# Performance work log

Hardware: AMD Instinct MI355X
Metric: run time of the kernel (lower is better)

Reference implementation:

```python
import jax, jax.numpy as jnp
import numpy as np

N = 50000      # nodes
E = 600000     # directed edges (before self-loops)
IN = 256       # in_channels
H = 4          # heads
C = 32         # hidden_channels (per head)
OUT = 64       # out_channels


def setup_inputs() -> dict:
    key = jax.random.key(0)
    ks = jax.random.split(key, 10)
    x = jax.random.normal(ks[0], (N, IN), dtype=jnp.float32)
    edge_index = jax.random.randint(ks[1], (2, E), 0, N, dtype=jnp.int64)
    W1 = jax.random.normal(ks[2], (IN, H * C), dtype=jnp.float32) / np.float32(np.sqrt(IN))
    a_src1 = jax.random.normal(ks[3], (H, C), dtype=jnp.float32) * 0.1
    a_dst1 = jax.random.normal(ks[4], (H, C), dtype=jnp.float32) * 0.1
    b1 = jnp.zeros((H * C,), dtype=jnp.float32)
    W2 = jax.random.normal(ks[5], (H * C, OUT), dtype=jnp.float32) / np.float32(np.sqrt(H * C))
    a_src2 = jax.random.normal(ks[6], (1, OUT), dtype=jnp.float32) * 0.1
    a_dst2 = jax.random.normal(ks[7], (1, OUT), dtype=jnp.float32) * 0.1
    b2 = jnp.zeros((OUT,), dtype=jnp.float32)
    return dict(x=x, edge_index=edge_index, W1=W1, a_src1=a_src1, a_dst1=a_dst1,
                b1=b1, W2=W2, a_src2=a_src2, a_dst2=a_dst2, b2=b2)


def gat_conv(x, src, dst, W, a_s, a_d, b, concat):
    """PyG GATConv (eval mode, self-loops already appended to src/dst).
    x: [N, F_in]; W: [F_in, H*C]; a_s, a_d: [H, C]; b: [H*C] or [C].
    Messages flow src (j) -> dst (i); softmax over incoming edges of dst."""
    heads, c = a_s.shape
    h = (x @ W).reshape(-1, heads, c)                      # [N, H, C]
    al_s = jnp.einsum('nhc,hc->nh', h, a_s)                # per-node src term
    al_d = jnp.einsum('nhc,hc->nh', h, a_d)                # per-node dst term
    e = jax.nn.leaky_relu(al_s[src] + al_d[dst], 0.2)      # [E, H]
    m = jax.ops.segment_max(e, dst, num_segments=N)        # stable segment softmax
    p = jnp.exp(e - m[dst])
    s = jax.ops.segment_sum(p, dst, num_segments=N)
    alpha = p / s[dst]                                     # [E, H]
    out = jax.ops.segment_sum(alpha[:, :, None] * h[src], dst, num_segments=N)  # [N, H, C]
    out = out.reshape(-1, heads * c) if concat else out.mean(axis=1)
    return out + b


def reference(x, edge_index, W1, a_src1, a_dst1, b1, W2, a_src2, a_dst2, b2):
    loops = jnp.arange(N, dtype=edge_index.dtype)          # PyG add_self_loops=True
    src = jnp.concatenate([edge_index[0], loops])
    dst = jnp.concatenate([edge_index[1], loops])
    h = gat_conv(x, src, dst, W1, a_src1, a_dst1, b1, concat=True)
    h = jax.nn.leaky_relu(h, 0.2)
    return gat_conv(h, src, dst, W2, a_src2, a_dst2, b2, concat=False)
```

## Files before the change

### kernel.cpp

```cpp
#include <hip/hip_runtime.h>
#include <hip/hip_bf16.h>

#define N_NODES 50000
#define E_EDGES 600000
#define F_IN    256
#define HC1     128
#define F_OUT   64
#define NBKT    196
#define BMAX    6144
#define APB     8192
#define NAB     80
#define GB1     1563
#define NPACK   (F_IN * HC1 + HC1 * F_OUT)

typedef __bf16 bf16x8 __attribute__((ext_vector_type(8)));
typedef __bf16 bf16x4 __attribute__((ext_vector_type(4)));
typedef float  f32x4  __attribute__((ext_vector_type(4)));

__device__ __forceinline__ float lrelu(float x) { return x > 0.f ? x : 0.2f * x; }
__device__ __forceinline__ float bfhi(unsigned v) { return __uint_as_float(v & 0xffff0000u); }
__device__ __forceinline__ float bflo(unsigned v) { return __uint_as_float(v << 16); }


__global__ __launch_bounds__(256) void init_kernel(const float* __restrict__ W1,
                                                   const float* __restrict__ W2,
                                                   __bf16* __restrict__ hi1, __bf16* __restrict__ lo1,
                                                   __bf16* __restrict__ hi2, __bf16* __restrict__ lo2,
                                                   int* __restrict__ bcur) {
    if (blockIdx.x == 0) {
        if (threadIdx.x < NBKT) bcur[threadIdx.x] = 0;
        return;
    }
    int tid = (blockIdx.x - 1) * 256 + threadIdx.x;
    if (tid >= NPACK) return;
    if (tid < F_IN * HC1) {
        int t = tid;
        int j = t & 7, l = (t >> 3) & 63, kt = (t >> 9) & 7, ct = t >> 12;
        int k = kt * 32 + (l >> 4) * 8 + j;
        int col = ct * 16 + (l & 15);
        float v = W1[k * HC1 + col];
        __bf16 h = (__bf16)v;
        hi1[t] = h;
        lo1[t] = (__bf16)(v - (float)h);
    } else {
        int t = tid - F_IN * HC1;
        int j = t & 7, l = (t >> 3) & 63, kt = (t >> 9) & 3, ct = t >> 11;
        int k = kt * 32 + (l >> 4) * 8 + j;
        int col = ct * 16 + (l & 15);
        float v = W2[k * F_OUT + col];
        __bf16 h = (__bf16)v;
        hi2[t] = h;
        lo2[t] = (__bf16)(v - (float)h);
    }
}


__global__ __launch_bounds__(256) void gemm1_bappend_kernel(
        const float* __restrict__ A,
        const __bf16* __restrict__ Whi, const __bf16* __restrict__ Wlo,
        const float* __restrict__ a_s, const float* __restrict__ a_d,
        __bf16* __restrict__ Cout, float* __restrict__ als, float* __restrict__ ald,
        const int* __restrict__ ei, int* __restrict__ bcur, int2* __restrict__ bstage) {
    __shared__ __bf16 ah[32][F_IN + 8];
    __shared__ __bf16 al[32][F_IN + 8];
    __shared__ int lcnt[NBKT];
    int tid = threadIdx.x;

    if (blockIdx.x < NAB) {
        const int TOT = E_EDGES + N_NODES;
        int bb = (int)blockIdx.x;
        int e0 = bb * APB;
        int e1 = e0 + APB < TOT ? e0 + APB : TOT;
        if (tid < NBKT) lcnt[tid] = 0;
        __syncthreads();
        for (int i = e0 + tid; i < e1; i += 256) {
            int d = (i < E_EDGES) ? ei[E_EDGES + i] : (i - E_EDGES);
            atomicAdd(&lcnt[d >> 8], 1);
        }
        __syncthreads();
        if (tid < NBKT) {
            int c = lcnt[tid];
            lcnt[tid] = c ? atomicAdd(&bcur[tid], c) : 0;
        }
        __syncthreads();
        for (int i = e0 + tid; i < e1; i += 256) {
            int s, d;
            if (i < E_EDGES) { s = ei[i]; d = ei[E_EDGES + i]; }
            else             { s = d = i - E_EDGES; }
            int b = d >> 8;
            int pos = atomicAdd(&lcnt[b], 1);
            bstage[(size_t)b * BMAX + pos] = make_int2(s, d);
        }
        return;
    }

    constexpr int KT = 8, CTW = 4, F4PR = 64;
    int tb = (int)blockIdx.x - NAB;
    #pragma unroll
    for (int it = 0; it < 8; ++it) {
        int idx = it * 256 + tid;
        int row = idx / F4PR;
        int kk  = (idx - row * F4PR) * 4;
        int grow = tb * 32 + row;
        const float* src = A + (size_t)(grow < N_NODES ? grow : N_NODES - 1) * F_IN + kk;
        float4 v = *(const float4*)src;
        bf16x4 h, lo;
        h[0] = (__bf16)v.x; h[1] = (__bf16)v.y; h[2] = (__bf16)v.z; h[3] = (__bf16)v.w;
        lo[0] = (__bf16)(v.x - (float)h[0]);
        lo[1] = (__bf16)(v.y - (float)h[1]);
        lo[2] = (__bf16)(v.z - (float)h[2]);
        lo[3] = (__bf16)(v.w - (float)h[3]);
        *(bf16x4*)&ah[row][kk] = h;
        *(bf16x4*)&al[row][kk] = lo;
    }
    __syncthreads();

    int w = tid >> 6, l = tid & 63;
    int rw = w & 1, cg = w >> 1;
    int c0 = cg * CTW;
    int r0 = tb * 32 + rw * 16;
    int rowL = rw * 16 + (l & 15);
    int koff = (l >> 4) * 8;

    bf16x8 bh[2][CTW], bl[2][CTW];
    #pragma unroll
    for (int c = 0; c < CTW; ++c) {
        size_t bidx = ((size_t)((c0 + c) * KT + 0) * 64 + l) * 8;
        bh[0][c] = *(const bf16x8*)(Whi + bidx);
        bl[0][c] = *(const bf16x8*)(Wlo + bidx);
    }

    f32x4 acc[CTW];
    #pragma unroll
    for (int c = 0; c < CTW; ++c) acc[c] = (f32x4){0.f, 0.f, 0.f, 0.f};

    #pragma unroll
    for (int kt = 0; kt < KT; ++kt) {
        const int cur = kt & 1, nxt = cur ^ 1;
        if (kt + 1 < KT) {
            #pragma unroll
            for (int c = 0; c < CTW; ++c) {
                size_t bidx = ((size_t)((c0 + c) * KT + (kt + 1)) * 64 + l) * 8;
                bh[nxt][c] = *(const bf16x8*)(Whi + bidx);
                bl[nxt][c] = *(const bf16x8*)(Wlo + bidx);
            }
        }
        bf16x8 ahi = *(const bf16x8*)&ah[rowL][kt * 32 + koff];
        bf16x8 alo = *(const bf16x8*)&al[rowL][kt * 32 + koff];
        #pragma unroll
        for (int c = 0; c < CTW; ++c) {
            acc[c] = __builtin_amdgcn_mfma_f32_16x16x32_bf16(ahi, bh[cur][c], acc[c], 0, 0, 0);
            acc[c] = __builtin_amdgcn_mfma_f32_16x16x32_bf16(ahi, bl[cur][c], acc[c], 0, 0, 0);
            acc[c] = __builtin_amdgcn_mfma_f32_16x16x32_bf16(alo, bh[cur][c], acc[c], 0, 0, 0);
        }
    }

    int crow0 = r0 + (l >> 4) * 4;
    int ccol = l & 15;

    #pragma unroll
    for (int c = 0; c < CTW; ++c) {
        #pragma unroll
        for (int r = 0; r < 4; ++r) {
            int row = crow0 + r;
            if (row < N_NODES)
                Cout[(size_t)row * HC1 + (c0 + c) * 16 + ccol] = (__bf16)acc[c][r];
        }
    }

    float as_c[CTW], ad_c[CTW];
    #pragma unroll
    for (int c = 0; c < CTW; ++c) {
        as_c[c] = a_s[(c0 + c) * 16 + ccol];
        ad_c[c] = a_d[(c0 + c) * 16 + ccol];
    }

    #pragma unroll
    for (int r = 0; r < 4; ++r) {
        int row = crow0 + r;
        #pragma unroll
        for (int hl = 0; hl < 2; ++hl) {
            int h = cg * 2 + hl;
            float vs = acc[2 * hl][r] * as_c[2 * hl] + acc[2 * hl + 1][r] * as_c[2 * hl + 1];
            float vd = acc[2 * hl][r] * ad_c[2 * hl] + acc[2 * hl + 1][r] * ad_c[2 * hl + 1];
            #pragma unroll
            for (int d = 1; d < 16; d <<= 1) {
                vs += __shfl_xor(vs, d);
                vd += __shfl_xor(vd, d);
            }
            if (ccol == 0 && row < N_NODES) { als[row * 4 + h] = vs; ald[row * 4 + h] = vd; }
        }
    }
}


__global__ __launch_bounds__(1024) void bsortp1_kernel(const int* __restrict__ bcur,
                                                       const int2* __restrict__ bstage,
                                                       const float* __restrict__ als1,
                                                       const float* __restrict__ ald1,
                                                       int* __restrict__ rowp,
                                                       int2* __restrict__ epair,
                                                       float* __restrict__ p1) {
    __shared__ int cnt[256], cur[256], ws4[4];
    __shared__ int bbase_s;
    __shared__ int2 sorted[BMAX];
    int b = blockIdx.x, tid = threadIdx.x;
    int nb = bcur[b]; if (nb > BMAX) nb = BMAX;
    int d0 = b << 8;

    if (tid < 256) {
        int lane = tid & 63, w = tid >> 6;
        int v = (tid < NBKT) ? bcur[tid] : 0;
        int s = v;
        #pragma unroll
        for (int d = 1; d < 64; d <<= 1) {
            int t = __shfl_up(s, d);
            if (lane >= d) s += t;
        }
        if (lane == 63) ws4[w] = s;
        __syncthreads();
        if (tid == 0) {
            int r = 0;
            #pragma unroll
            for (int q = 0; q < 4; ++q) { int t = ws4[q]; ws4[q] = r; r += t; }
        }
        __syncthreads();
        if (tid == b) bbase_s = ws4[w] + s - v;
        if (b == 0 && tid == 0) rowp[N_NODES] = E_EDGES + N_NODES;
    } else {
        __syncthreads();
        __syncthreads();
    }
    if (tid < 256) cnt[tid] = 0;
    __syncthreads();
    int base = bbase_s;

    const int2* bs = bstage + (size_t)b * BMAX;
    for (int e = tid; e < nb; e += 1024)
        atomicAdd(&cnt[bs[e].y - d0], 1);
    __syncthreads();
    int v = 0, s = 0;
    if (tid < 256) {
        int lane = tid & 63, w = tid >> 6;
        v = cnt[tid];
        s = v;
        #pragma unroll
        for (int d = 1; d < 64; d <<= 1) {
            int t = __shfl_up(s, d);
            if (lane >= d) s += t;
        }
        if (lane == 63) ws4[w] = s;
    }
    __syncthreads();
    if (tid == 0) {
        int r = 0;
        #pragma unroll
        for (int q = 0; q < 4; ++q) { int t = ws4[q]; ws4[q] = r; r += t; }
    }
    __syncthreads();
    if (tid < 256) {
        int excl = ws4[tid >> 6] + s - v;
        cur[tid] = excl;
        int d = d0 + tid;
        if (d < N_NODES) rowp[d] = base + excl;
    }
    __syncthreads();
    for (int e = tid; e < nb; e += 1024) {
        int2 ed = bs[e];
        int p = atomicAdd(&cur[ed.y - d0], 1);
        sorted[p] = ed;
    }
    __syncthreads();
    for (int e = tid; e < nb; e += 1024) {
        int2 ed = sorted[e];
        epair[base + e] = ed;
        float4 as = *(const float4*)&als1[ed.x * 4];
        float4 ad = *(const float4*)&ald1[ed.y * 4];
        float4 p;
        p.x = __expf(lrelu(as.x + ad.x));
        p.y = __expf(lrelu(as.y + ad.y));
        p.z = __expf(lrelu(as.z + ad.z));
        p.w = __expf(lrelu(as.w + ad.w));
        *(float4*)&p1[(size_t)(base + e) * 4] = p;
    }
}


template<int KDIM, int NC, bool CBF16, int CGROUPS>
__global__ __launch_bounds__(256) void gemm_mfma_kernel(const float* __restrict__ A,
                                                        const __bf16* __restrict__ Whi,
                                                        const __bf16* __restrict__ Wlo,
                                                        const float* __restrict__ a_s,
                                                        const float* __restrict__ a_d,
                                                        void* __restrict__ Cout,
                                                        float* __restrict__ als,
                                                        float* __restrict__ ald) {
    constexpr int KT   = KDIM / 32;
    constexpr int CT   = NC / 16;
    constexpr int CTW  = CT / CGROUPS;
    constexpr int RPB  = (CGROUPS == 2) ? 32 : 64;
    constexpr int LSTR = KDIM + 8;
    constexpr int F4PR = KDIM / 4;
    __shared__ __bf16 ah[RPB][LSTR];
    __shared__ __bf16 al[RPB][LSTR];

    int tid = threadIdx.x;

    #pragma unroll
    for (int it = 0; it < (RPB * F4PR) / 256; ++it) {
        int idx = it * 256 + tid;
        int row = idx / F4PR;
        int kk  = (idx - row * F4PR) * 4;
        int grow = blockIdx.x * RPB + row;
        const float* src = A + (size_t)(grow < N_NODES ? grow : N_NODES - 1) * KDIM + kk;
        float4 v = *(const float4*)src;
        bf16x4 h, lo;
        h[0] = (__bf16)v.x; h[1] = (__bf16)v.y; h[2] = (__bf16)v.z; h[3] = (__bf16)v.w;
        lo[0] = (__bf16)(v.x - (float)h[0]);
        lo[1] = (__bf16)(v.y - (float)h[1]);
        lo[2] = (__bf16)(v.z - (float)h[2]);
        lo[3] = (__bf16)(v.w - (float)h[3]);
        *(bf16x4*)&ah[row][kk] = h;
        *(bf16x4*)&al[row][kk] = lo;
    }
    __syncthreads();

    int w = tid >> 6, l = tid & 63;
    int rw = (CGROUPS == 2) ? (w & 1) : w;
    int cg = (CGROUPS == 2) ? (w >> 1) : 0;
    int c0 = cg * CTW;
    int r0 = blockIdx.x * RPB + rw * 16;
    int rowL = rw * 16 + (l & 15);
    int koff = (l >> 4) * 8;

    bf16x8 bh[2][CTW], bl[2][CTW];
    #pragma unroll
    for (int c = 0; c < CTW; ++c) {
        size_t bidx = ((size_t)((c0 + c) * KT + 0) * 64 + l) * 8;
        bh[0][c] = *(const bf16x8*)(Whi + bidx);
        bl[0][c] = *(const bf16x8*)(Wlo + bidx);
    }

    f32x4 acc[CTW];
    #pragma unroll
    for (int c = 0; c < CTW; ++c) acc[c] = (f32x4){0.f, 0.f, 0.f, 0.f};

    #pragma unroll
    for (int kt = 0; kt < KT; ++kt) {
        const int cur = kt & 1, nxt = cur ^ 1;
        if (kt + 1 < KT) {
            #pragma unroll
            for (int c = 0; c < CTW; ++c) {
                size_t bidx = ((size_t)((c0 + c) * KT + (kt + 1)) * 64 + l) * 8;
                bh[nxt][c] = *(const bf16x8*)(Whi + bidx);
                bl[nxt][c] = *(const bf16x8*)(Wlo + bidx);
            }
        }
        bf16x8 ahi = *(const bf16x8*)&ah[rowL][kt * 32 + koff];
        bf16x8 alo = *(const bf16x8*)&al[rowL][kt * 32 + koff];
        #pragma unroll
        for (int c = 0; c < CTW; ++c) {
            acc[c] = __builtin_amdgcn_mfma_f32_16x16x32_bf16(ahi, bh[cur][c], acc[c], 0, 0, 0);
            acc[c] = __builtin_amdgcn_mfma_f32_16x16x32_bf16(ahi, bl[cur][c], acc[c], 0, 0, 0);
            acc[c] = __builtin_amdgcn_mfma_f32_16x16x32_bf16(alo, bh[cur][c], acc[c], 0, 0, 0);
        }
    }

    int crow0 = r0 + (l >> 4) * 4;
    int ccol = l & 15;

    #pragma unroll
    for (int c = 0; c < CTW; ++c) {
        #pragma unroll
        for (int r = 0; r < 4; ++r) {
            int row = crow0 + r;
            if (row < N_NODES) {
                if constexpr (CBF16)
                    ((__bf16*)Cout)[(size_t)row * NC + (c0 + c) * 16 + ccol] = (__bf16)acc[c][r];
                else
                    ((float*)Cout)[(size_t)row * NC + (c0 + c) * 16 + ccol] = acc[c][r];
            }
        }
    }

    float as_c[CTW], ad_c[CTW];
    #pragma unroll
    for (int c = 0; c < CTW; ++c) {
        as_c[c] = a_s[(c0 + c) * 16 + ccol];
        ad_c[c] = a_d[(c0 + c) * 16 + ccol];
    }

    #pragma unroll
    for (int r = 0; r < 4; ++r) {
        int row = crow0 + r;
        if constexpr (NC == 128) {
            #pragma unroll
            for (int hl = 0; hl < 2; ++hl) {
                int h = cg * 2 + hl;
                float vs = acc[2 * hl][r] * as_c[2 * hl] + acc[2 * hl + 1][r] * as_c[2 * hl + 1];
                float vd = acc[2 * hl][r] * ad_c[2 * hl] + acc[2 * hl + 1][r] * ad_c[2 * hl + 1];
                #pragma unroll
                for (int d = 1; d < 16; d <<= 1) {
                    vs += __shfl_xor(vs, d);
                    vd += __shfl_xor(vd, d);
                }
                if (ccol == 0 && row < N_NODES) { als[row * 4 + h] = vs; ald[row * 4 + h] = vd; }
            }
        } else {
            float vs = 0.f, vd = 0.f;
            #pragma unroll
            for (int c = 0; c < CTW; ++c) { vs += acc[c][r] * as_c[c]; vd += acc[c][r] * ad_c[c]; }
            #pragma unroll
            for (int d = 1; d < 16; d <<= 1) {
                vs += __shfl_xor(vs, d);
                vd += __shfl_xor(vd, d);
            }
            if (ccol == 0 && row < N_NODES) { als[row] = vs; ald[row] = vd; }
        }
    }
}


__global__ __launch_bounds__(256) void aggr1_kernel(const int* __restrict__ row_ptr,
                                                    const int2* __restrict__ epair,
                                                    const float* __restrict__ p1,
                                                    const __bf16* __restrict__ h1b,
                                                    const float* __restrict__ b1,
                                                    float* __restrict__ h2out) {
    int wid = blockIdx.x * 4 + (threadIdx.x >> 6);
    int lane = threadIdx.x & 63;
    int grp = lane >> 4, li = lane & 15;
    int hh = li >> 2;
    int beg = row_ptr[wid], end = row_ptr[wid + 1];
    float acc[8] = {0,0,0,0,0,0,0,0};
    float S = 0.f;
    for (int j0 = beg; j0 < end; j0 += 4) {
        int j = j0 + grp;
        bool valid = (j < end);
        int s = valid ? epair[j].x : 0;
        float p = valid ? p1[(size_t)j * 4 + hh] : 0.f;
        uint4 v = *(const uint4*)(h1b + (size_t)s * HC1 + li * 8);
        acc[0] += p * bflo(v.x); acc[1] += p * bfhi(v.x);
        acc[2] += p * bflo(v.y); acc[3] += p * bfhi(v.y);
        acc[4] += p * bflo(v.z); acc[5] += p * bfhi(v.z);
        acc[6] += p * bflo(v.w); acc[7] += p * bfhi(v.w);
        S += p;
    }
    #pragma unroll
    for (int d = 16; d < 64; d <<= 1) {
        #pragma unroll
        for (int c = 0; c < 8; ++c) acc[c] += __shfl_xor(acc[c], d);
        S += __shfl_xor(S, d);
    }
    if (grp == 0) {
        float inv = 1.f / S;
        const float* bp = b1 + li * 8;
        float4 o0, o1;
        o0.x = lrelu(acc[0] * inv + bp[0]);
        o0.y = lrelu(acc[1] * inv + bp[1]);
        o0.z = lrelu(acc[2] * inv + bp[2]);
        o0.w = lrelu(acc[3] * inv + bp[3]);
        o1.x = lrelu(acc[4] * inv + bp[4]);
        o1.y = lrelu(acc[5] * inv + bp[5]);
        o1.z = lrelu(acc[6] * inv + bp[6]);
        o1.w = lrelu(acc[7] * inv + bp[7]);
        float* orow = h2out + (size_t)wid * HC1 + li * 8;
        *(float4*)orow = o0;
        *(float4*)(orow + 4) = o1;
    }
}

__global__ __launch_bounds__(256) void aggr2_kernel(const int* __restrict__ row_ptr,
                                                    const int2* __restrict__ epair,
                                                    const float* __restrict__ als2,
                                                    const float* __restrict__ ald2,
                                                    const float* __restrict__ g,
                                                    const float* __restrict__ b2,
                                                    float* __restrict__ out) {
    int wid = blockIdx.x * 4 + (threadIdx.x >> 6);
    int lane = threadIdx.x & 63;
    int grp = lane >> 4, li = lane & 15;
    int beg = row_ptr[wid], end = row_ptr[wid + 1];
    float ad = ald2[wid];
    float a0 = 0.f, a1 = 0.f, a2 = 0.f, a3 = 0.f, S = 0.f;
    for (int j0 = beg; j0 < end; j0 += 4) {
        int j = j0 + grp;
        bool valid = (j < end);
        int s = valid ? epair[j].x : 0;
        float p = valid ? __expf(lrelu(als2[s] + ad)) : 0.f;
        float4 gv = *(const float4*)(g + (size_t)s * F_OUT + li * 4);
        a0 += p * gv.x; a1 += p * gv.y; a2 += p * gv.z; a3 += p * gv.w;
        S += p;
    }
    #pragma unroll
    for (int d = 16; d < 64; d <<= 1) {
        a0 += __shfl_xor(a0, d); a1 += __shfl_xor(a1, d);
        a2 += __shfl_xor(a2, d); a3 += __shfl_xor(a3, d);
        S += __shfl_xor(S, d);
    }
    if (grp == 0) {
        float inv = 1.f / S;
        const float* bp = b2 + li * 4;
        float4 o;
        o.x = a0 * inv + bp[0];
        o.y = a1 * inv + bp[1];
        o.z = a2 * inv + bp[2];
        o.w = a3 * inv + bp[3];
        *(float4*)(out + (size_t)wid * F_OUT + li * 4) = o;
    }
}


extern "C" void kernel_launch(void* const* d_in, const int* in_sizes, int n_in,
                              void* d_out, int out_size, void* d_ws, size_t ws_size,
                              hipStream_t stream) {
    const float* x      = (const float*)d_in[0];
    const int*   ei     = (const int*)  d_in[1];
    const float* W1     = (const float*)d_in[2];
    const float* a_src1 = (const float*)d_in[3];
    const float* a_dst1 = (const float*)d_in[4];
    const float* b1     = (const float*)d_in[5];
    const float* W2     = (const float*)d_in[6];
    const float* a_src2 = (const float*)d_in[7];
    const float* a_dst2 = (const float*)d_in[8];
    const float* b2     = (const float*)d_in[9];
    float* out = (float*)d_out;
    char* ws = (char*)d_ws;

    __bf16* h1b    = (__bf16*)(ws + 0);
    float* h2      = (float*)(ws + 12800000);
    float* g       = (float*)(ws + 38400000);
    float* als1    = (float*)(ws + 51200000);
    float* ald1    = (float*)(ws + 52000000);
    float* als2    = (float*)(ws + 52800000);
    float* ald2    = (float*)(ws + 53000000);
    int*   rowp    = (int*)  (ws + 53200000);
    int*   bcur    = (int*)  (ws + 53400064);
    int2*  bstage  = (int2*) (ws + 53402112);
    int2*  epair   = (int2*) (ws + 63035904);
    __bf16* whi1   = (__bf16*)(ws + 68235904);
    __bf16* wlo1   = (__bf16*)(ws + 68301440);
    __bf16* whi2   = (__bf16*)(ws + 68366976);
    __bf16* wlo2   = (__bf16*)(ws + 68383360);
    float* p1 = g;

    init_kernel<<<1 + (NPACK + 255) / 256, 256, 0, stream>>>(
        W1, W2, whi1, wlo1, whi2, wlo2, bcur);

    gemm1_bappend_kernel<<<NAB + GB1, 256, 0, stream>>>(
        x, whi1, wlo1, a_src1, a_dst1, h1b, als1, ald1, ei, bcur, bstage);

    bsortp1_kernel<<<NBKT, 1024, 0, stream>>>(bcur, bstage, als1, ald1, rowp, epair, p1);

    aggr1_kernel<<<N_NODES / 4, 256, 0, stream>>>(rowp, epair, p1, h1b, b1, h2);

    gemm_mfma_kernel<HC1, F_OUT, false, 1><<<(N_NODES + 63) / 64, 256, 0, stream>>>(
        h2, whi2, wlo2, a_src2, a_dst2, g, als2, ald2);

    aggr2_kernel<<<N_NODES / 4, 256, 0, stream>>>(rowp, epair, als2, ald2, g, b2, out);
}
```

Measured before the change: 138.7 us.

## Fuse layer-1 aggregation with layer-2 GEMM through shared memory

Merges the layer-1 aggregation kernel and the layer-2 MFMA GEMM into one kernel. Each 1024-thread block aggregates 16 nodes, stores the activated rows as bf16 hi/lo pairs in LDS, then four waves compute the 16x64 projection and the attention logits. This removes the fp32 h2 intermediate write and reread, plus one launch. In exchange, 12 of 16 waves sit idle during the GEMM phase, each block reloads the W2 fragments, and the large blocks with barriers may reduce occupancy. p1 moves to its own buffer because g is now written while p1 is still being read.

```diff
diff --git a/kernel.cpp b/kernel.cpp
--- a/kernel.cpp
+++ b/kernel.cpp
@@ -286,152 +286,23 @@
 }
 
 
-template<int KDIM, int NC, bool CBF16, int CGROUPS>
-__global__ __launch_bounds__(256) void gemm_mfma_kernel(const float* __restrict__ A,
-                                                        const __bf16* __restrict__ Whi,
-                                                        const __bf16* __restrict__ Wlo,
-                                                        const float* __restrict__ a_s,
-                                                        const float* __restrict__ a_d,
-                                                        void* __restrict__ Cout,
-                                                        float* __restrict__ als,
-                                                        float* __restrict__ ald) {
-    constexpr int KT   = KDIM / 32;
-    constexpr int CT   = NC / 16;
-    constexpr int CTW  = CT / CGROUPS;
-    constexpr int RPB  = (CGROUPS == 2) ? 32 : 64;
-    constexpr int LSTR = KDIM + 8;
-    constexpr int F4PR = KDIM / 4;
-    __shared__ __bf16 ah[RPB][LSTR];
-    __shared__ __bf16 al[RPB][LSTR];
-
+__global__ __launch_bounds__(1024) void aggr1g_kernel(
+        const int* __restrict__ rowp, const int2* __restrict__ epair,
+        const float* __restrict__ p1, const __bf16* __restrict__ h1b,
+        const float* __restrict__ b1,
+        const __bf16* __restrict__ whi2, const __bf16* __restrict__ wlo2,
+        const float* __restrict__ a_src2, const float* __restrict__ a_dst2,
+        float* __restrict__ g, float* __restrict__ als2, float* __restrict__ ald2) {
+    __shared__ __bf16 h2h[16][HC1 + 8];
+    __shared__ __bf16 h2l[16][HC1 + 8];
+    __shared__ float alsp[4][16], aldp[4][16];
     int tid = threadIdx.x;
-
-    #pragma unroll
-    for (int it = 0; it < (RPB * F4PR) / 256; ++it) {
-        int idx = it * 256 + tid;
-        int row = idx / F4PR;
-        int kk  = (idx - row * F4PR) * 4;
-        int grow = blockIdx.x * RPB + row;
-        const float* src = A + (size_t)(grow < N_NODES ? grow : N_NODES - 1) * KDIM + kk;
-        float4 v = *(const float4*)src;
-        bf16x4 h, lo;
-        h[0] = (__bf16)v.x; h[1] = (__bf16)v.y; h[2] = (__bf16)v.z; h[3] = (__bf16)v.w;
-        lo[0] = (__bf16)(v.x - (float)h[0]);
-        lo[1] = (__bf16)(v.y - (float)h[1]);
-        lo[2] = (__bf16)(v.z - (float)h[2]);
-        lo[3] = (__bf16)(v.w - (float)h[3]);
-        *(bf16x4*)&ah[row][kk] = h;
-        *(bf16x4*)&al[row][kk] = lo;
-    }
-    __syncthreads();
-
     int w = tid >> 6, l = tid & 63;
-    int rw = (CGROUPS == 2) ? (w & 1) : w;
-    int cg = (CGROUPS == 2) ? (w >> 1) : 0;
-    int c0 = cg * CTW;
-    int r0 = blockIdx.x * RPB + rw * 16;
-    int rowL = rw * 16 + (l & 15);
-    int koff = (l >> 4) * 8;
-
-    bf16x8 bh[2][CTW], bl[2][CTW];
-    #pragma unroll
-    for (int c = 0; c < CTW; ++c) {
-        size_t bidx = ((size_t)((c0 + c) * KT + 0) * 64 + l) * 8;
-        bh[0][c] = *(const bf16x8*)(Whi + bidx);
-        bl[0][c] = *(const bf16x8*)(Wlo + bidx);
-    }
-
-    f32x4 acc[CTW];
-    #pragma unroll
-    for (int c = 0; c < CTW; ++c) acc[c] = (f32x4){0.f, 0.f, 0.f, 0.f};
-
-    #pragma unroll
-    for (int kt = 0; kt < KT; ++kt) {
-        const int cur = kt & 1, nxt = cur ^ 1;
-        if (kt + 1 < KT) {
-            #pragma unroll
-            for (int c = 0; c < CTW; ++c) {
-                size_t bidx = ((size_t)((c0 + c) * KT + (kt + 1)) * 64 + l) * 8;
-                bh[nxt][c] = *(const bf16x8*)(Whi + bidx);
-                bl[nxt][c] = *(const bf16x8*)(Wlo + bidx);
-            }
-        }
-        bf16x8 ahi = *(const bf16x8*)&ah[rowL][kt * 32 + koff];
-        bf16x8 alo = *(const bf16x8*)&al[rowL][kt * 32 + koff];
-        #pragma unroll
-        for (int c = 0; c < CTW; ++c) {
-            acc[c] = __builtin_amdgcn_mfma_f32_16x16x32_bf16(ahi, bh[cur][c], acc[c], 0, 0, 0);
-            acc[c] = __builtin_amdgcn_mfma_f32_16x16x32_bf16(ahi, bl[cur][c], acc[c], 0, 0, 0);
-            acc[c] = __builtin_amdgcn_mfma_f32_16x16x32_bf16(alo, bh[cur][c], acc[c], 0, 0, 0);
-        }
-    }
-
-    int crow0 = r0 + (l >> 4) * 4;
-    int ccol = l & 15;
-
-    #pragma unroll
-    for (int c = 0; c < CTW; ++c) {
-        #pragma unroll
-        for (int r = 0; r < 4; ++r) {
-            int row = crow0 + r;
-            if (row < N_NODES) {
-                if constexpr (CBF16)
-                    ((__bf16*)Cout)[(size_t)row * NC + (c0 + c) * 16 + ccol] = (__bf16)acc[c][r];
-                else
-                    ((float*)Cout)[(size_t)row * NC + (c0 + c) * 16 + ccol] = acc[c][r];
-            }
-        }
-    }
-
-    float as_c[CTW], ad_c[CTW];
-    #pragma unroll
-    for (int c = 0; c < CTW; ++c) {
-        as_c[c] = a_s[(c0 + c) * 16 + ccol];
-        ad_c[c] = a_d[(c0 + c) * 16 + ccol];
-    }
-
-    #pragma unroll
-    for (int r = 0; r < 4; ++r) {
-        int row = crow0 + r;
-        if constexpr (NC == 128) {
-            #pragma unroll
-            for (int hl = 0; hl < 2; ++hl) {
-                int h = cg * 2 + hl;
-                float vs = acc[2 * hl][r] * as_c[2 * hl] + acc[2 * hl + 1][r] * as_c[2 * hl + 1];
-                float vd = acc[2 * hl][r] * ad_c[2 * hl] + acc[2 * hl + 1][r] * ad_c[2 * hl + 1];
-                #pragma unroll
-                for (int d = 1; d < 16; d <<= 1) {
-                    vs += __shfl_xor(vs, d);
-                    vd += __shfl_xor(vd, d);
-                }
-                if (ccol == 0 && row < N_NODES) { als[row * 4 + h] = vs; ald[row * 4 + h] = vd; }
-            }
-        } else {
-            float vs = 0.f, vd = 0.f;
-            #pragma unroll
-            for (int c = 0; c < CTW; ++c) { vs += acc[c][r] * as_c[c]; vd += acc[c][r] * ad_c[c]; }
-            #pragma unroll
-            for (int d = 1; d < 16; d <<= 1) {
-                vs += __shfl_xor(vs, d);
-                vd += __shfl_xor(vd, d);
-            }
-            if (ccol == 0 && row < N_NODES) { als[row] = vs; ald[row] = vd; }
-        }
-    }
-}
-
-
-__global__ __launch_bounds__(256) void aggr1_kernel(const int* __restrict__ row_ptr,
-                                                    const int2* __restrict__ epair,
-                                                    const float* __restrict__ p1,
-                                                    const __bf16* __restrict__ h1b,
-                                                    const float* __restrict__ b1,
-                                                    float* __restrict__ h2out) {
-    int wid = blockIdx.x * 4 + (threadIdx.x >> 6);
-    int lane = threadIdx.x & 63;
-    int grp = lane >> 4, li = lane & 15;
+    int wid = blockIdx.x * 16 + w;
+    int grp = l >> 4, li = l & 15;
     int hh = li >> 2;
-    int beg = row_ptr[wid], end = row_ptr[wid + 1];
+    int beg = rowp[wid], end = rowp[wid + 1];
+
     float acc[8] = {0,0,0,0,0,0,0,0};
     float S = 0.f;
     for (int j0 = beg; j0 < end; j0 += 4) {
@@ -455,20 +326,64 @@
     if (grp == 0) {
         float inv = 1.f / S;
         const float* bp = b1 + li * 8;
-        float4 o0, o1;
-        o0.x = lrelu(acc[0] * inv + bp[0]);
-        o0.y = lrelu(acc[1] * inv + bp[1]);
-        o0.z = lrelu(acc[2] * inv + bp[2]);
-        o0.w = lrelu(acc[3] * inv + bp[3]);
-        o1.x = lrelu(acc[4] * inv + bp[4]);
-        o1.y = lrelu(acc[5] * inv + bp[5]);
-        o1.z = lrelu(acc[6] * inv + bp[6]);
-        o1.w = lrelu(acc[7] * inv + bp[7]);
-        float* orow = h2out + (size_t)wid * HC1 + li * 8;
-        *(float4*)orow = o0;
-        *(float4*)(orow + 4) = o1;
-    }
-}
+        bf16x8 hv, lv;
+        #pragma unroll
+        for (int c = 0; c < 8; ++c) {
+            float o = lrelu(acc[c] * inv + bp[c]);
+            __bf16 h = (__bf16)o;
+            hv[c] = h;
+            lv[c] = (__bf16)(o - (float)h);
+        }
+        *(bf16x8*)&h2h[w][li * 8] = hv;
+        *(bf16x8*)&h2l[w][li * 8] = lv;
+    }
+    __syncthreads();
+
+    if (w < 4) {
+        constexpr int KT = 4;
+        int c0 = w;
+        bf16x8 bh[KT], bl[KT];
+        #pragma unroll
+        for (int kt = 0; kt < KT; ++kt) {
+            size_t bidx = ((size_t)(c0 * KT + kt) * 64 + l) * 8;
+            bh[kt] = *(const bf16x8*)(whi2 + bidx);
+            bl[kt] = *(const bf16x8*)(wlo2 + bidx);
+        }
+        int ar = l & 15, koff = (l >> 4) * 8;
+        f32x4 acc2 = (f32x4){0.f, 0.f, 0.f, 0.f};
+        #pragma unroll
+        for (int kt = 0; kt < KT; ++kt) {
+            bf16x8 ahi = *(const bf16x8*)&h2h[ar][kt * 32 + koff];
+            bf16x8 alo = *(const bf16x8*)&h2l[ar][kt * 32 + koff];
+            acc2 = __builtin_amdgcn_mfma_f32_16x16x32_bf16(ahi, bh[kt], acc2, 0, 0, 0);
+            acc2 = __builtin_amdgcn_mfma_f32_16x16x32_bf16(ahi, bl[kt], acc2, 0, 0, 0);
+            acc2 = __builtin_amdgcn_mfma_f32_16x16x32_bf16(alo, bh[kt], acc2, 0, 0, 0);
+        }
+        int crow0 = (l >> 4) * 4;
+        int ccol = l & 15;
+        float as_c = a_src2[c0 * 16 + ccol];
+        float ad_c = a_dst2[c0 * 16 + ccol];
+        #pragma unroll
+        for (int r = 0; r < 4; ++r) {
+            int row = blockIdx.x * 16 + crow0 + r;
+            g[(size_t)row * F_OUT + c0 * 16 + ccol] = acc2[r];
+            float vs = acc2[r] * as_c;
+            float vd = acc2[r] * ad_c;
+            #pragma unroll
+            for (int d = 1; d < 16; d <<= 1) {
+                vs += __shfl_xor(vs, d);
+                vd += __shfl_xor(vd, d);
+            }
+            if (ccol == 0) { alsp[c0][crow0 + r] = vs; aldp[c0][crow0 + r] = vd; }
+        }
+    }
+    __syncthreads();
+    if (tid < 16) {
+        als2[blockIdx.x * 16 + tid] = alsp[0][tid] + alsp[1][tid] + alsp[2][tid] + alsp[3][tid];
+        ald2[blockIdx.x * 16 + tid] = aldp[0][tid] + aldp[1][tid] + aldp[2][tid] + aldp[3][tid];
+    }
+}
+
 
 __global__ __launch_bounds__(256) void aggr2_kernel(const int* __restrict__ row_ptr,
                                                     const int2* __restrict__ epair,
@@ -528,7 +443,7 @@
     char* ws = (char*)d_ws;
 
     __bf16* h1b    = (__bf16*)(ws + 0);
-    float* h2      = (float*)(ws + 12800000);
+    float* p1      = (float*)(ws + 12800000);
     float* g       = (float*)(ws + 38400000);
     float* als1    = (float*)(ws + 51200000);
     float* ald1    = (float*)(ws + 52000000);
@@ -542,7 +457,6 @@
     __bf16* wlo1   = (__bf16*)(ws + 68301440);
     __bf16* whi2   = (__bf16*)(ws + 68366976);
     __bf16* wlo2   = (__bf16*)(ws + 68383360);
-    float* p1 = g;
 
     init_kernel<<<1 + (NPACK + 255) / 256, 256, 0, stream>>>(
         W1, W2, whi1, wlo1, whi2, wlo2, bcur);
@@ -552,10 +466,8 @@
 
     bsortp1_kernel<<<NBKT, 1024, 0, stream>>>(bcur, bstage, als1, ald1, rowp, epair, p1);
 
-    aggr1_kernel<<<N_NODES / 4, 256, 0, stream>>>(rowp, epair, p1, h1b, b1, h2);
-
-    gemm_mfma_kernel<HC1, F_OUT, false, 1><<<(N_NODES + 63) / 64, 256, 0, stream>>>(
-        h2, whi2, wlo2, a_src2, a_dst2, g, als2, ald2);
+    aggr1g_kernel<<<N_NODES / 16, 1024, 0, stream>>>(
+        rowp, epair, p1, h1b, b1, whi2, wlo2, a_src2, a_dst2, g, als2, ald2);
 
     aggr2_kernel<<<N_NODES / 4, 256, 0, stream>>>(rowp, epair, als2, ald2, g, b2, out);
 }
```

Result: no change. 137.9 us (-0.6%).
